# Performance work log

Measured on AMD Instinct MI355X. Metric: run time of the kernel, lower is better.

The kernel has to match this reference:

```python
import jax, jax.numpy as jnp
import numpy as np

B, CIN, COUT, H, W, K, S, P = 16, 256, 128, 64, 64, 4, 2, 1
PAD = K - 1 - P  # transposed-conv equivalent padding for the lhs-dilated conv


def setup_inputs() -> dict:
    key = jax.random.key(0)
    ks = jax.random.split(key, 13)
    return {
        "x": jax.random.normal(ks[0], (B, CIN, H, W), jnp.float32),
        "feature": jax.random.uniform(ks[1], (B, 4), jnp.float32),
        "weight": jax.random.normal(ks[2], (CIN, COUT, K, K), jnp.float32) * 0.05,
        "t_bayer": jax.random.normal(ks[3], (1, CIN, COUT, K, K), jnp.float32) * 0.05,
        "t_quad": jax.random.normal(ks[4], (1, CIN, COUT, K, K), jnp.float32) * 0.05,
        "t_nano": jax.random.normal(ks[5], (1, CIN, COUT, K, K), jnp.float32) * 0.05,
        "t_qxq": jax.random.normal(ks[6], (1, CIN, COUT, K, K), jnp.float32) * 0.05,
        "m_bayer": jax.random.uniform(ks[7], (1, CIN, COUT, 1, 1), jnp.float32),
        "m_quad": jax.random.uniform(ks[8], (1, CIN, COUT, 1, 1), jnp.float32),
        "m_nano": jax.random.uniform(ks[9], (1, CIN, COUT, 1, 1), jnp.float32),
        "m_qxq": jax.random.uniform(ks[10], (1, CIN, COUT, 1, 1), jnp.float32),
        "bias": jax.random.normal(ks[11], (COUT,), jnp.float32) * 0.05,
        "prelu_a": jnp.full((1,), 0.25, jnp.float32),
    }


def _synth_weights(feature, weight, t_bayer, t_quad, t_nano, t_qxq,
                   m_bayer, m_quad, m_nano, m_qxq):
    # feature: (B,4) softmax attention -> (B,4,1,1,1)
    sa = feature[:, :, None, None, None]
    dyn = (t_bayer * m_bayer * sa[:, 0:1]
           + t_quad * m_quad * sa[:, 1:2]
           + t_nano * m_nano * sa[:, 2:3]
           + t_qxq * m_qxq * sa[:, 3:4])  # (B, CIN, COUT, K, K)
    return weight[None] + dyn  # broadcast base weight over batch


def _deconv_per_sample(xi, wi):
    # xi: (CIN,H,W); wi: (CIN,COUT,K,K) torch conv_transpose layout.
    # conv_transpose == lhs-dilated conv with spatially-flipped, transposed kernel
    kern = jnp.flip(jnp.swapaxes(wi, 0, 1), axis=(-2, -1))  # (COUT,CIN,K,K)
    out = jax.lax.conv_general_dilated(
        xi[None], kern, window_strides=(1, 1),
        padding=[(PAD, PAD), (PAD, PAD)], lhs_dilation=(S, S),
        dimension_numbers=("NCHW", "OIHW", "NCHW"))
    return out[0]  # (COUT, H*S, W*S)


def reference(x, feature, weight, t_bayer, t_quad, t_nano, t_qxq,
              m_bayer, m_quad, m_nano, m_qxq, bias, prelu_a):
    w = _synth_weights(feature, weight, t_bayer, t_quad, t_nano, t_qxq,
                       m_bayer, m_quad, m_nano, m_qxq)
    out = jax.vmap(_deconv_per_sample)(x, w)  # (B, COUT, 128, 128)
    out = out + bias[None, :, None, None]
    # PReLU with single shared slope (torch default init 0.25)
    return jnp.where(out >= 0, out, prelu_a[0] * out)
```

## Files before the change

kernel.cpp:

```cpp
#include <hip/hip_runtime.h>
#include <hip/hip_bf16.h>
#include <cstddef>
#include <cstdint>

#define B_    16
#define CIN_  256
#define COUT_ 128
#define H_    64
#define W_    64
#define OH_   128
#define OW_   128

#define AST   44
#define ACHUNK (128*AST)

typedef __attribute__((ext_vector_type(8))) short bf16x8;
typedef __attribute__((ext_vector_type(4))) float f32x4;

__device__ inline short f2bf(float f) {
    __hip_bfloat16 h = __float2bfloat16(f);
    return *reinterpret_cast<short*>(&h);
}

__device__ inline void async_ld16(const void* g, void* l) {
    typedef const __attribute__((address_space(1))) unsigned int* gp_t;
    typedef __attribute__((address_space(3))) unsigned int* lp_t;
    __builtin_amdgcn_global_load_lds((gp_t)g, (lp_t)l, 16, 0, 0);
}

__device__ inline void synth_body(
    int chunk, int cog8, int tid,
    const float* __restrict__ weight,
    const float* __restrict__ tb, const float* __restrict__ tq,
    const float* __restrict__ tn, const float* __restrict__ tx,
    const float* __restrict__ mb, const float* __restrict__ mq,
    const float* __restrict__ mn, const float* __restrict__ mx,
    const float* __restrict__ feat,
    short* __restrict__ aws,
    short* lbuf )
{
    const int ci_l = tid >> 5;
    const int co_l = (tid >> 2) & 7;
    const int kh   = tid & 3;
    const int base = (chunk*8 + ci_l) * COUT_ + cog8*8 + co_l;

    const float4 w4 = *(const float4*)(weight + (size_t)base*16 + kh*4);
    const float4 b4 = *(const float4*)(tb + (size_t)base*16 + kh*4);
    const float4 q4 = *(const float4*)(tq + (size_t)base*16 + kh*4);
    const float4 n4 = *(const float4*)(tn + (size_t)base*16 + kh*4);
    const float4 x4 = *(const float4*)(tx + (size_t)base*16 + kh*4);
    const float m_b = mb[base], m_q = mq[base];
    const float m_n = mn[base], m_x = mx[base];
    const float* wp = (const float*)&w4;
    const float* bp = (const float*)&b4;
    const float* qp = (const float*)&q4;
    const float* np = (const float*)&n4;
    const float* xp = (const float*)&x4;

    const int r  = (kh+1)&1;
    const int dh = (kh<2) ? 1 : 0;

    const int o_cls = tid >> 6;
    const int o_cor = (tid >> 3) & 7;
    const int o_e8  = tid & 7;

    for (int b = 0; b < 16; ++b) {
        const float sb = m_b * feat[b*4+0];
        const float sq = m_q * feat[b*4+1];
        const float sn = m_n * feat[b*4+2];
        const float sx = m_x * feat[b*4+3];
        #pragma unroll
        for (int kw = 0; kw < 4; ++kw) {
            int s  = (kw+1)&1;
            int dw = (kw<2) ? 1 : 0;
            float v = wp[kw] + sb*bp[kw] + sq*qp[kw] + sn*np[kw] + sx*xp[kw];
            lbuf[((r*2+s)*8 + co_l)*32 + (dh*2+dw)*8 + ci_l] = f2bf(v);
        }
        __syncthreads();
        {
            size_t row = ((((size_t)(b*4 + o_cls)*32 + chunk)*128)
                          + cog8*8 + o_cor);
            *(int2*)(aws + row*AST + o_e8*4) =
                *(const int2*)(lbuf + (o_cls*8 + o_cor)*32 + o_e8*4);
        }
        __syncthreads();
    }
}

__device__ inline void transform_body(
    int ihp, int b, int tid,
    const float* __restrict__ x, short* __restrict__ xt,
    float* xls )
{
    const int4 z4 = {0, 0, 0, 0};

    if (ihp == 0 || ihp == 65) {
        for (int j = tid; j < 2112; j += 256) {
            int c = j / 66, iwp = j - c*66;
            *(int4*)(xt + ((((size_t)b*32 + c)*66 + ihp)*66 + iwp)*8) = z4;
        }
        return;
    }
    if (tid < 64) {
        int c = tid >> 1, iwp = (tid & 1) * 65;
        *(int4*)(xt + ((((size_t)b*32 + c)*66 + ihp)*66 + iwp)*8) = z4;
    }
    const int ih = ihp - 1;
    for (int half = 0; half < 2; ++half) {
        __syncthreads();
        #pragma unroll
        for (int it = 0; it < 8; ++it) {
            int ci_l = it*16 + (tid >> 4);
            int iw4  = (tid & 15) * 4;
            float4 v = *(const float4*)(
                x + (((size_t)b*256 + half*128 + ci_l)*64 + ih)*64 + iw4);
            *(float4*)(xls + ci_l*68 + iw4) = v;
        }
        __syncthreads();
        #pragma unroll
        for (int it2 = 0; it2 < 4; ++it2) {
            int chunk_l = it2*4 + (tid >> 6);
            int chunk   = half*16 + chunk_l;
            int iw      = tid & 63;
            short s8[8];
            #pragma unroll
            for (int j = 0; j < 8; ++j)
                s8[j] = f2bf(xls[(chunk_l*8 + j)*68 + iw]);
            *(int4*)(xt + ((((size_t)b*32 + chunk)*66 + ihp)*66 + (iw+1))*8)
                = *(const int4*)s8;
        }
    }
}

__global__ __launch_bounds__(256) void prep_fused(
    const float* __restrict__ x,
    const float* __restrict__ weight,
    const float* __restrict__ tb, const float* __restrict__ tq,
    const float* __restrict__ tn, const float* __restrict__ tx,
    const float* __restrict__ mb, const float* __restrict__ mq,
    const float* __restrict__ mn, const float* __restrict__ mx,
    const float* __restrict__ feat,
    short* __restrict__ aws, short* __restrict__ xt)
{
    __shared__ __align__(16) char smem[34816];
    const int bid = blockIdx.x;
    const int tid = threadIdx.x;
    if (bid < 1056) {
        int ihp = bid % 66, b = bid / 66;
        transform_body(ihp, b, tid, x, xt, (float*)smem);
    } else {
        int sb = bid - 1056;
        int chunk = sb & 31, cog8 = sb >> 5;
        synth_body(chunk, cog8, tid, weight, tb, tq, tn, tx,
                   mb, mq, mn, mx, feat, aws, (short*)smem);
    }
}

__global__ __launch_bounds__(256) void synth_aws(
    const float* __restrict__ weight,
    const float* __restrict__ tb, const float* __restrict__ tq,
    const float* __restrict__ tn, const float* __restrict__ tx,
    const float* __restrict__ mb, const float* __restrict__ mq,
    const float* __restrict__ mn, const float* __restrict__ mx,
    const float* __restrict__ feat,
    short* __restrict__ aws)
{
    __shared__ __align__(16) short lbuf[4][8][32];
    synth_body(blockIdx.x, blockIdx.y, threadIdx.x, weight, tb, tq, tn, tx,
               mb, mq, mn, mx, feat, aws, &lbuf[0][0][0]);
}

__global__ __launch_bounds__(256, 2) void deconv_mfma4(
    const short* __restrict__ aws, const short* __restrict__ xt,
    const float* __restrict__ bias, const float* __restrict__ prelu_a,
    float* __restrict__ out)
{
    const int tid  = threadIdx.x;
    const int lane = tid & 63;
    const int wv   = tid >> 6;
    const int wm   = wv & 1, wn = wv >> 1;
    const int o    = blockIdx.x;
    const int x8   = o & 7;
    const int l    = o >> 3;
    const int cls  = l & 3;
    const int nt2  = (l >> 2) & 15;
    const int b    = 2*x8 + (l >> 6);
    const int a0 = (nt2 >> 1) * 8, c0 = (nt2 & 1) * 32;
    const int r = cls >> 1, s = cls & 1;

    __shared__ __align__(16) short als[2][ACHUNK];
    __shared__ __align__(16) short xsb[2][2560];

    const short* gb[4]; size_t gstep[4]; int loff[4], isB[4];
    {
        const size_t awb = (((size_t)b*4 + cls)*32) * ACHUNK;
        #pragma unroll
        for (int i = 0; i < 4; ++i) {
            int t = wv + i*4;
            if (t < 11) {
                gb[i]    = aws + awb + t*512 + lane*8;
                gstep[i] = ACHUNK;  loff[i] = t*512;  isB[i] = 0;
            } else {
                int j = t - 11;
                int p = j*64 + lane; if (p > 296) p = 296;
                int row = p / 33, col = p - row*33;
                gb[i] = xt + (((size_t)b*32*66 + (a0 + r + row))*66
                              + (c0 + s + col)) * 8;
                gstep[i] = 66*66*8;  loff[i] = j*512;  isB[i] = 1;
            }
        }
    }

    f32x4 acc[4][8];
    #pragma unroll
    for (int mi = 0; mi < 4; ++mi)
        #pragma unroll
        for (int ni = 0; ni < 8; ++ni)
            acc[mi][ni] = (f32x4){0.f, 0.f, 0.f, 0.f};

    const int nlo = lane & 15;
    const int q   = lane >> 4;
    const int dh  = q >> 1, dw = q & 1;

    #pragma unroll
    for (int i = 0; i < 4; ++i)
        async_ld16(gb[i], isB[i] ? &xsb[0][loff[i]] : &als[0][loff[i]]);

    for (int c = 0; c < 32; ++c) {
        __syncthreads();
        const int sel = c & 1;
        if (c < 31) {
            const int ps = sel ^ 1;
            #pragma unroll
            for (int i = 0; i < 4; ++i)
                async_ld16(gb[i] + (size_t)(c+1)*gstep[i],
                           isB[i] ? &xsb[ps][loff[i]] : &als[ps][loff[i]]);
        }
        bf16x8 af[4], bfr[8];
        #pragma unroll
        for (int mi = 0; mi < 4; ++mi)
            af[mi] = *(const bf16x8*)(&als[sel][(wm*64 + mi*16 + nlo)*AST + q*8]);
        #pragma unroll
        for (int ni = 0; ni < 8; ++ni) {
            int a_local = wn*4 + (ni & 3);
            int colx    = nlo + (ni >> 2)*16 + dw;
            bfr[ni] = *(const bf16x8*)(&xsb[sel][((a_local + dh)*33 + colx)*8]);
        }
        #pragma unroll
        for (int mi = 0; mi < 4; ++mi)
            #pragma unroll
            for (int ni = 0; ni < 8; ++ni)
                acc[mi][ni] = __builtin_amdgcn_mfma_f32_16x16x32_bf16(
                    af[mi], bfr[ni], acc[mi][ni], 0, 0, 0);
    }

    const float pa = prelu_a[0];
    #pragma unroll
    for (int mi = 0; mi < 4; ++mi) {
        #pragma unroll
        for (int reg = 0; reg < 4; ++reg) {
            int co = wm*64 + mi*16 + q*4 + reg;
            float bv = bias[co];
            #pragma unroll
            for (int ni = 0; ni < 8; ++ni) {
                int a_local = wn*4 + (ni & 3);
                int cg      = ni >> 2;
                int oh = 2*(a0 + a_local) + r;
                int ow = 2*(c0 + cg*16 + nlo) + s;
                float v = acc[mi][ni][reg] + bv;
                v = (v >= 0.f) ? v : pa*v;
                out[(((size_t)b*COUT_ + co)*OH_ + oh)*OW_ + ow] = v;
            }
        }
    }
}

__global__ __launch_bounds__(256, 2) void deconv_mfma_gather(
    const float* __restrict__ x,
    const short* __restrict__ aws,
    const float* __restrict__ bias,
    const float* __restrict__ prelu_a,
    float* __restrict__ out)
{
    const int tid  = threadIdx.x;
    const int lane = tid & 63;
    const int wv   = tid >> 6;
    const int wm   = wv & 1, wn = wv >> 1;
    const int nt   = blockIdx.x;
    const int cls  = blockIdx.y;
    const int b    = blockIdx.z;
    const int a0 = (nt >> 2) * 8, c0 = (nt & 3) * 16;
    const int r = cls >> 1, s = cls & 1;

    __shared__ __align__(16) short xs[1280];

    int goff[5], gstep[5], gok[5];
    #pragma unroll
    for (int i = 0; i < 5; ++i) {
        int e    = tid + i*256;
        int ci_l = e & 7;
        int rc   = e >> 3;
        int row  = rc / 17;
        int col  = rc - row*17;
        int ih   = a0 - 1 + r + row;
        int iw   = c0 - 1 + s + col;
        int ok   = (rc < 153) && ((unsigned)ih < (unsigned)H_)
                              && ((unsigned)iw < (unsigned)W_);
        goff[i]  = ok ? (((b*CIN_ + ci_l)*H_ + ih)*W_ + iw) : 0;
        gstep[i] = ok ? (8*H_*W_) : 0;
        gok[i]   = ok;
    }
    const int nlo = lane & 15;
    const int q   = lane >> 4;
    const int dh  = q >> 1, dw = q & 1;

    const size_t awb = (((size_t)b*4 + cls)*32) * ACHUNK;
    const short* agp = aws + awb + (wm*64 + nlo)*AST + q*8;

    f32x4 acc[4][4];
    #pragma unroll
    for (int mi = 0; mi < 4; ++mi)
        #pragma unroll
        for (int ni = 0; ni < 4; ++ni)
            acc[mi][ni] = (f32x4){0.f, 0.f, 0.f, 0.f};

    for (int chunk = 0; chunk < 32; ++chunk) {
        __syncthreads();
        #pragma unroll
        for (int i = 0; i < 5; ++i) {
            float v = x[goff[i] + chunk*gstep[i]];
            v = gok[i] ? v : 0.0f;
            xs[tid + i*256] = f2bf(v);
        }
        bf16x8 af[4];
        #pragma unroll
        for (int mi = 0; mi < 4; ++mi) {
            const short* p = agp + (size_t)chunk*ACHUNK + mi*16*AST;
            union { int2 h[2]; bf16x8 v; } u;
            u.h[0] = *(const int2*)p;
            u.h[1] = *(const int2*)(p + 4);
            af[mi] = u.v;
        }
        __syncthreads();
        bf16x8 bfr[4];
        #pragma unroll
        for (int ni = 0; ni < 4; ++ni) {
            int a_local = wn*4 + ni;
            bfr[ni] = *(const bf16x8*)(xs + ((a_local + dh)*17 + (nlo + dw))*8);
        }
        #pragma unroll
        for (int mi = 0; mi < 4; ++mi)
            #pragma unroll
            for (int ni = 0; ni < 4; ++ni)
                acc[mi][ni] = __builtin_amdgcn_mfma_f32_16x16x32_bf16(
                    af[mi], bfr[ni], acc[mi][ni], 0, 0, 0);
    }

    const float pa = prelu_a[0];
    #pragma unroll
    for (int mi = 0; mi < 4; ++mi) {
        #pragma unroll
        for (int reg = 0; reg < 4; ++reg) {
            int co = wm*64 + mi*16 + q*4 + reg;
            float bv = bias[co];
            #pragma unroll
            for (int ni = 0; ni < 4; ++ni) {
                int a_local = wn*4 + ni;
                int oh = 2*(a0 + a_local) + r;
                int ow = 2*(c0 + nlo) + s;
                float v = acc[mi][ni][reg] + bv;
                v = (v >= 0.f) ? v : pa*v;
                out[(((size_t)b*COUT_ + co)*OH_ + oh)*OW_ + ow] = v;
            }
        }
    }
}

__global__ __launch_bounds__(256) void deconv_fallback(
    const float* __restrict__ x,
    const float* __restrict__ weight,
    const float* __restrict__ tb, const float* __restrict__ tq,
    const float* __restrict__ tn, const float* __restrict__ tx,
    const float* __restrict__ mb, const float* __restrict__ mq,
    const float* __restrict__ mn, const float* __restrict__ mx,
    const float* __restrict__ feat,
    const float* __restrict__ bias, const float* __restrict__ prelu_a,
    float* __restrict__ out)
{
    const int tid    = threadIdx.x;
    const int tile   = blockIdx.x;
    const int coT    = blockIdx.y;
    const int b      = blockIdx.z;
    const int tile_h = tile >> 3, tile_w = tile & 7;
    const int a0 = tile_h * 8;
    const int c0 = tile_w * 8;
    const int co0 = coT * 64;

    const int tco = tid & 15;
    const int tpx = tid >> 4;
    const int rr  = tpx >> 2, rc = tpx & 3;

    __shared__ float xsf[4][100];
    __shared__ float wsh[4][16][64];

    float acc[4][4][4];
    #pragma unroll
    for (int i = 0; i < 4; ++i)
        #pragma unroll
        for (int j = 0; j < 4; ++j)
            #pragma unroll
            for (int c = 0; c < 4; ++c) acc[i][j][c] = 0.f;

    float f0 = feat[b*4 + 0], f1 = feat[b*4 + 1];
    float f2 = feat[b*4 + 2], f3 = feat[b*4 + 3];

    for (int chunk = 0; chunk < CIN_ / 4; ++chunk) {
        const int ci0 = chunk * 4;
        __syncthreads();
        for (int e = tid; e < 400; e += 256) {
            int ci_l = e / 100; int rem = e - ci_l * 100;
            int rI = rem / 10;  int cI = rem - rI * 10;
            int ih = a0 - 1 + rI, iw = c0 - 1 + cI;
            float v = 0.f;
            if ((unsigned)ih < (unsigned)H_ && (unsigned)iw < (unsigned)W_)
                v = x[(((size_t)b * CIN_ + ci0 + ci_l) * H_ + ih) * W_ + iw];
            xsf[ci_l][rem] = v;
        }
        #pragma unroll
        for (int k = 0; k < 4; ++k) {
            int g = tid + k * 256;
            int ci_l = g >> 8; int rrem = g & 255;
            int co_l = rrem >> 2; int tg = (rrem & 3) * 4;
            int cico = (ci0 + ci_l) * COUT_ + co0 + co_l;
            int e = cico * 16 + tg;
            float4 w  = *(const float4*)(weight + e);
            float4 vb = *(const float4*)(tb + e);
            float4 vq = *(const float4*)(tq + e);
            float4 vn = *(const float4*)(tn + e);
            float4 vx = *(const float4*)(tx + e);
            float sb = mb[cico] * f0, sq = mq[cico] * f1;
            float sn = mn[cico] * f2, sx = mx[cico] * f3;
            float4 wvv;
            wvv.x = w.x + sb*vb.x + sq*vq.x + sn*vn.x + sx*vx.x;
            wvv.y = w.y + sb*vb.y + sq*vq.y + sn*vn.y + sx*vx.y;
            wvv.z = w.z + sb*vb.z + sq*vq.z + sn*vn.z + sx*vx.z;
            wvv.w = w.w + sb*vb.w + sq*vq.w + sn*vn.w + sx*vx.w;
            wsh[ci_l][tg + 0][co_l] = wvv.x;
            wsh[ci_l][tg + 1][co_l] = wvv.y;
            wsh[ci_l][tg + 2][co_l] = wvv.z;
            wsh[ci_l][tg + 3][co_l] = wvv.w;
        }
        __syncthreads();
        #pragma unroll
        for (int ci_l = 0; ci_l < 4; ++ci_l) {
            float xpv[4][4];
            #pragma unroll
            for (int i = 0; i < 4; ++i)
                #pragma unroll
                for (int j = 0; j < 4; ++j)
                    xpv[i][j] = xsf[ci_l][(rr*2 + i) * 10 + rc*2 + j];
            #pragma unroll
            for (int kh = 0; kh < 4; ++kh) {
                const int rpar = (kh & 1) ? 0 : 1;
                const int offh = (kh == 0) ? 2 : (kh == 3) ? 0 : 1;
                #pragma unroll
                for (int kw = 0; kw < 4; ++kw) {
                    const int spar = (kw & 1) ? 0 : 1;
                    const int offw = (kw == 0) ? 2 : (kw == 3) ? 0 : 1;
                    float4 wvv = *(const float4*)&wsh[ci_l][kh*4 + kw][tco*4];
                    float wr[4] = {wvv.x, wvv.y, wvv.z, wvv.w};
                    #pragma unroll
                    for (int da = 0; da < 2; ++da)
                        #pragma unroll
                        for (int dc = 0; dc < 2; ++dc) {
                            const float xvv = xpv[da + offh][dc + offw];
                            #pragma unroll
                            for (int cc = 0; cc < 4; ++cc)
                                acc[2*da + rpar][2*dc + spar][cc] =
                                    fmaf(wr[cc], xvv, acc[2*da + rpar][2*dc + spar][cc]);
                        }
                }
            }
        }
    }
    const float pa  = prelu_a[0];
    const int oh0 = tile_h * 16 + rr * 4;
    const int ow0 = tile_w * 16 + rc * 4;
    #pragma unroll
    for (int cc = 0; cc < 4; ++cc) {
        const int co = co0 + tco * 4 + cc;
        const float bv = bias[co];
        #pragma unroll
        for (int dr = 0; dr < 4; ++dr)
            #pragma unroll
            for (int dw2 = 0; dw2 < 4; ++dw2) {
                float v = acc[dr][dw2][cc] + bv;
                v = (v >= 0.f) ? v : pa * v;
                out[(((size_t)b * COUT_ + co) * OH_ + (oh0 + dr)) * OW_ + (ow0 + dw2)] = v;
            }
    }
}

extern "C" void kernel_launch(void* const* d_in, const int* in_sizes, int n_in,
                              void* d_out, int out_size, void* d_ws, size_t ws_size,
                              hipStream_t stream) {
    (void)in_sizes; (void)n_in; (void)out_size;
    const float* x      = (const float*)d_in[0];
    const float* feat   = (const float*)d_in[1];
    const float* weight = (const float*)d_in[2];
    const float* tb     = (const float*)d_in[3];
    const float* tq     = (const float*)d_in[4];
    const float* tn     = (const float*)d_in[5];
    const float* tx     = (const float*)d_in[6];
    const float* mb     = (const float*)d_in[7];
    const float* mq     = (const float*)d_in[8];
    const float* mn     = (const float*)d_in[9];
    const float* mx     = (const float*)d_in[10];
    const float* bias   = (const float*)d_in[11];
    const float* prelu  = (const float*)d_in[12];
    float* out = (float*)d_out;

    const size_t aws_sz = (size_t)B_ * 4 * 32 * 128 * AST * sizeof(short);
    const size_t xt_sz  = (size_t)B_ * 32 * 66 * 66 * 8 * sizeof(short);

    if (ws_size >= aws_sz + xt_sz) {
        short* aws = (short*)d_ws;
        short* xt  = (short*)((char*)d_ws + aws_sz);
        prep_fused<<<dim3(1056 + 512), 256, 0, stream>>>(
            x, weight, tb, tq, tn, tx, mb, mq, mn, mx, feat, aws, xt);
        deconv_mfma4<<<dim3(1024), 256, 0, stream>>>(
            aws, xt, bias, prelu, out);
    } else if (ws_size >= aws_sz) {
        short* aws = (short*)d_ws;
        synth_aws<<<dim3(32, 16), 256, 0, stream>>>(
            weight, tb, tq, tn, tx, mb, mq, mn, mx, feat, aws);
        deconv_mfma_gather<<<dim3(32, 4, 16), 256, 0, stream>>>(
            x, aws, bias, prelu, out);
    } else {
        deconv_fallback<<<dim3(64, 2, 16), 256, 0, stream>>>(
            x, weight, tb, tq, tn, tx, mb, mq, mn, mx, feat, bias, prelu, out);
    }
}
```

Measured before the change: 289.1 us.

## Swizzle weight chunks unpadded and double K-step per pipeline stage

Replaces the padded 44-element row stride of the synthesized weight chunks with a dense 64-byte row layout that XOR-swizzles 16-byte columns by row, avoiding LDS bank conflicts without padding. The main MFMA kernel now loads two CIN chunks per double-buffered stage (16 iterations instead of 32), halving barrier count and issuing more async loads per stage. LDS use per block roughly doubles, which could limit occupancy at two blocks per CU; the gather fallback is updated to read the new layout.

```diff
diff --git a/kernel.cpp b/kernel.cpp
--- a/kernel.cpp
+++ b/kernel.cpp
@@ -11,8 +11,7 @@
 #define OH_   128
 #define OW_   128
 
-#define AST   44
-#define ACHUNK (128*AST)
+#define ACH   4096
 
 typedef __attribute__((ext_vector_type(8))) short bf16x8;
 typedef __attribute__((ext_vector_type(4))) float f32x4;
@@ -63,6 +62,7 @@
     const int o_cls = tid >> 6;
     const int o_cor = (tid >> 3) & 7;
     const int o_e8  = tid & 7;
+    const int o_off = (((cog8*8 + o_cor)*64 + o_e8*8) ^ (o_cor << 4));
 
     for (int b = 0; b < 16; ++b) {
         const float sb = m_b * feat[b*4+0];
@@ -78,9 +78,8 @@
         }
         __syncthreads();
         {
-            size_t row = ((((size_t)(b*4 + o_cls)*32 + chunk)*128)
-                          + cog8*8 + o_cor);
-            *(int2*)(aws + row*AST + o_e8*4) =
+            size_t sbase = ((size_t)(b*4 + o_cls)*32 + chunk) * ACH;
+            *(int2*)(aws + sbase + (o_off >> 1)) =
                 *(const int2*)(lbuf + (o_cls*8 + o_cor)*32 + o_e8*4);
         }
         __syncthreads();
@@ -170,7 +169,7 @@
                mb, mq, mn, mx, feat, aws, &lbuf[0][0][0]);
 }
 
-__global__ __launch_bounds__(256, 2) void deconv_mfma4(
+__global__ __launch_bounds__(256, 2) void deconv_mfma6(
     const short* __restrict__ aws, const short* __restrict__ xt,
     const float* __restrict__ bias, const float* __restrict__ prelu_a,
     float* __restrict__ out)
@@ -188,25 +187,28 @@
     const int a0 = (nt2 >> 1) * 8, c0 = (nt2 & 1) * 32;
     const int r = cls >> 1, s = cls & 1;
 
-    __shared__ __align__(16) short als[2][ACHUNK];
-    __shared__ __align__(16) short xsb[2][2560];
-
-    const short* gb[4]; size_t gstep[4]; int loff[4], isB[4];
+    __shared__ __align__(16) short als[2][2*ACH];
+    __shared__ __align__(16) short xsb[2][2*2560];
+
+    const short* gb[7]; size_t gstep[7]; int loff[7], isB[7], act[7];
     {
-        const size_t awb = (((size_t)b*4 + cls)*32) * ACHUNK;
-        #pragma unroll
-        for (int i = 0; i < 4; ++i) {
+        const size_t awb = (((size_t)b*4 + cls)*32) * ACH;
+        #pragma unroll
+        for (int i = 0; i < 7; ++i) {
             int t = wv + i*4;
-            if (t < 11) {
-                gb[i]    = aws + awb + t*512 + lane*8;
-                gstep[i] = ACHUNK;  loff[i] = t*512;  isB[i] = 0;
+            act[i] = (t < 26);
+            if (t < 16) {
+                int half = t >> 3, u = t & 7;
+                gb[i]    = aws + awb + half*ACH + u*512 + lane*8;
+                gstep[i] = 2*ACH;  loff[i] = half*4096 + u*512;  isB[i] = 0;
             } else {
-                int j = t - 11;
-                int p = j*64 + lane; if (p > 296) p = 296;
+                int j = t - 16; if (j > 9) j = 9;
+                int half = (j >= 5) ? 1 : 0, jj = j - half*5;
+                int p = jj*64 + lane; if (p > 296) p = 296;
                 int row = p / 33, col = p - row*33;
-                gb[i] = xt + (((size_t)b*32*66 + (a0 + r + row))*66
+                gb[i] = xt + (((size_t)(b*32 + half)*66 + (a0 + r + row))*66
                               + (c0 + s + col)) * 8;
-                gstep[i] = 66*66*8;  loff[i] = j*512;  isB[i] = 1;
+                gstep[i] = 2*66*66*8;  loff[i] = half*2560 + jj*512;  isB[i] = 1;
             }
         }
     }
@@ -222,36 +224,50 @@
     const int q   = lane >> 4;
     const int dh  = q >> 1, dw = q & 1;
 
-    #pragma unroll
-    for (int i = 0; i < 4; ++i)
-        async_ld16(gb[i], isB[i] ? &xsb[0][loff[i]] : &als[0][loff[i]]);
-
-    for (int c = 0; c < 32; ++c) {
+    int aoff[4];
+    #pragma unroll
+    for (int mi = 0; mi < 4; ++mi) {
+        int row  = wm*64 + mi*16 + nlo;
+        aoff[mi] = ((row*64 + q*16) ^ ((nlo & 7) << 4)) >> 1;
+    }
+
+    #pragma unroll
+    for (int i = 0; i < 7; ++i)
+        if (act[i])
+            async_ld16(gb[i], isB[i] ? &xsb[0][loff[i]] : &als[0][loff[i]]);
+
+    for (int c = 0; c < 16; ++c) {
         __syncthreads();
         const int sel = c & 1;
-        if (c < 31) {
+        if (c < 15) {
             const int ps = sel ^ 1;
             #pragma unroll
-            for (int i = 0; i < 4; ++i)
-                async_ld16(gb[i] + (size_t)(c+1)*gstep[i],
-                           isB[i] ? &xsb[ps][loff[i]] : &als[ps][loff[i]]);
-        }
-        bf16x8 af[4], bfr[8];
-        #pragma unroll
-        for (int mi = 0; mi < 4; ++mi)
-            af[mi] = *(const bf16x8*)(&als[sel][(wm*64 + mi*16 + nlo)*AST + q*8]);
-        #pragma unroll
-        for (int ni = 0; ni < 8; ++ni) {
-            int a_local = wn*4 + (ni & 3);
-            int colx    = nlo + (ni >> 2)*16 + dw;
-            bfr[ni] = *(const bf16x8*)(&xsb[sel][((a_local + dh)*33 + colx)*8]);
-        }
-        #pragma unroll
-        for (int mi = 0; mi < 4; ++mi)
-            #pragma unroll
-            for (int ni = 0; ni < 8; ++ni)
-                acc[mi][ni] = __builtin_amdgcn_mfma_f32_16x16x32_bf16(
-                    af[mi], bfr[ni], acc[mi][ni], 0, 0, 0);
+            for (int i = 0; i < 7; ++i)
+                if (act[i])
+                    async_ld16(gb[i] + (size_t)(c+1)*gstep[i],
+                               isB[i] ? &xsb[ps][loff[i]] : &als[ps][loff[i]]);
+        }
+        #pragma unroll
+        for (int h = 0; h < 2; ++h) {
+            const short* ab = &als[sel][h*4096];
+            const short* xb = &xsb[sel][h*2560];
+            bf16x8 af[4], bfr[8];
+            #pragma unroll
+            for (int mi = 0; mi < 4; ++mi)
+                af[mi] = *(const bf16x8*)(ab + aoff[mi]);
+            #pragma unroll
+            for (int ni = 0; ni < 8; ++ni) {
+                int a_local = wn*4 + (ni & 3);
+                int colx    = nlo + (ni >> 2)*16 + dw;
+                bfr[ni] = *(const bf16x8*)(xb + ((a_local + dh)*33 + colx)*8);
+            }
+            #pragma unroll
+            for (int mi = 0; mi < 4; ++mi)
+                #pragma unroll
+                for (int ni = 0; ni < 8; ++ni)
+                    acc[mi][ni] = __builtin_amdgcn_mfma_f32_16x16x32_bf16(
+                        af[mi], bfr[ni], acc[mi][ni], 0, 0, 0);
+        }
     }
 
     const float pa = prelu_a[0];
@@ -314,8 +330,13 @@
     const int q   = lane >> 4;
     const int dh  = q >> 1, dw = q & 1;
 
-    const size_t awb = (((size_t)b*4 + cls)*32) * ACHUNK;
-    const short* agp = aws + awb + (wm*64 + nlo)*AST + q*8;
+    const size_t awb = (((size_t)b*4 + cls)*32) * ACH;
+    int aoff[4];
+    #pragma unroll
+    for (int mi = 0; mi < 4; ++mi) {
+        int row  = wm*64 + mi*16 + nlo;
+        aoff[mi] = ((row*64 + q*16) ^ ((nlo & 7) << 4)) >> 1;
+    }
 
     f32x4 acc[4][4];
     #pragma unroll
@@ -334,13 +355,8 @@
         }
         bf16x8 af[4];
         #pragma unroll
-        for (int mi = 0; mi < 4; ++mi) {
-            const short* p = agp + (size_t)chunk*ACHUNK + mi*16*AST;
-            union { int2 h[2]; bf16x8 v; } u;
-            u.h[0] = *(const int2*)p;
-            u.h[1] = *(const int2*)(p + 4);
-            af[mi] = u.v;
-        }
+        for (int mi = 0; mi < 4; ++mi)
+            af[mi] = *(const bf16x8*)(aws + awb + (size_t)chunk*ACH + aoff[mi]);
         __syncthreads();
         bf16x8 bfr[4];
         #pragma unroll
@@ -520,7 +536,7 @@
     const float* prelu  = (const float*)d_in[12];
     float* out = (float*)d_out;
 
-    const size_t aws_sz = (size_t)B_ * 4 * 32 * 128 * AST * sizeof(short);
+    const size_t aws_sz = (size_t)B_ * 4 * 32 * ACH * sizeof(short);
     const size_t xt_sz  = (size_t)B_ * 32 * 66 * 66 * 8 * sizeof(short);
 
     if (ws_size >= aws_sz + xt_sz) {
@@ -528,7 +544,7 @@
         short* xt  = (short*)((char*)d_ws + aws_sz);
         prep_fused<<<dim3(1056 + 512), 256, 0, stream>>>(
             x, weight, tb, tq, tn, tx, mb, mq, mn, mx, feat, aws, xt);
-        deconv_mfma4<<<dim3(1024), 256, 0, stream>>>(
+        deconv_mfma6<<<dim3(1024), 256, 0, stream>>>(
             aws, xt, bias, prelu, out);
     } else if (ws_size >= aws_sz) {
         short* aws = (short*)d_ws;
```

Result: faster. 279.3 us (-3.4%).
